# Kernel optimization log

Hardware: AMD Instinct MI355X
Metric: run time of the kernel (lower is better)

## Reference

```python
import jax, jax.numpy as jnp
import numpy as np

B, N, D_MODEL, N_HEADS = 4, 2048, 1024, 16
D_K = D_MODEL // N_HEADS  # 64


def setup_inputs() -> dict:
    key = jax.random.key(0)
    ks = jax.random.split(key, 7)
    s = 1.0 / np.sqrt(D_MODEL)
    return {
        "Q": jax.random.normal(ks[0], (B, N, D_MODEL), jnp.float32),
        "K": jax.random.normal(ks[1], (B, N, D_MODEL), jnp.float32),
        "V": jax.random.normal(ks[2], (B, N, D_MODEL), jnp.float32),
        "w_q": jax.random.normal(ks[3], (D_MODEL, D_MODEL), jnp.float32) * s,
        "w_k": jax.random.normal(ks[4], (D_MODEL, D_K), jnp.float32) * s,
        "w_v": jax.random.normal(ks[5], (D_MODEL, D_K), jnp.float32) * s,
        "w_o": jax.random.normal(ks[6], (D_MODEL, D_MODEL), jnp.float32) * s,
    }


def reference(Q, K, V, w_q, w_k, w_v, w_o):
    b, n, _ = Q.shape
    # projections: multi-query -> single shared K/V head of width d_k
    q = (Q @ w_q).reshape(b, n, N_HEADS, D_K)   # [b, n, h, d]
    k = K @ w_k                                  # [b, n, d]
    v = V @ w_v                                  # [b, n, d]
    scale = 1.0 / jnp.sqrt(jnp.asarray(D_K, q.dtype))
    scores = jnp.einsum("bnhd,bmd->bhnm", q, k) * scale  # [b, h, n, n]
    # causal mask: query i attends to keys j <= i (strictly-upper positions masked)
    causal = jnp.triu(jnp.ones((n, n), dtype=bool), k=1)
    scores = jnp.where(causal[None, None], -jnp.inf, scores)
    weights = jax.nn.softmax(scores, axis=-1)
    attn = jnp.einsum("bhnm,bmd->bnhd", weights, v).reshape(b, n, D_MODEL)
    return attn @ w_o
```

## Files before the change

### kernel.cpp

```cpp
#include <hip/hip_runtime.h>

typedef __bf16 bf16;
typedef unsigned int u32;
typedef __bf16 bf16x8 __attribute__((ext_vector_type(8)));
typedef float f32x4 __attribute__((ext_vector_type(4)));
typedef float f32x16 __attribute__((ext_vector_type(16)));

#define DEV __device__ __forceinline__

DEV void gload_lds16(const void* g, void* l) {
  __builtin_amdgcn_global_load_lds((const __attribute__((address_space(1))) void*)g,
                                   (__attribute__((address_space(3))) void*)l,
                                   16, 0, 0);
}

DEV u32 pack2(float a, float b) {
  unsigned short ua = __builtin_bit_cast(unsigned short, (bf16)a);
  unsigned short ub = __builtin_bit_cast(unsigned short, (bf16)b);
  return (u32)ua | ((u32)ub << 16);
}

__global__ void transpose_all(const float* __restrict__ wq, const float* __restrict__ wk,
                              const float* __restrict__ wv, const float* __restrict__ wo,
                              bf16* __restrict__ wqT, bf16* __restrict__ wkvT,
                              bf16* __restrict__ woT, float scale_q) {
  __shared__ float tile[32][33];
  int x = blockIdx.x;
  const float* in;
  bf16* out;
  int C;
  float scale = 1.0f;
  int c0;
  if (x < 32)      { in = wq; out = wqT;             C = 1024; c0 = x * 32; scale = scale_q; }
  else if (x < 34) { in = wk; out = wkvT;            C = 64;   c0 = (x - 32) * 32; }
  else if (x < 36) { in = wv; out = wkvT + 64 * 1024; C = 64;  c0 = (x - 34) * 32; }
  else             { in = wo; out = woT;             C = 1024; c0 = (x - 36) * 32; }
  int r0 = blockIdx.y * 32;
  int tx = threadIdx.x & 31, ty = threadIdx.x >> 5;
  for (int i = ty; i < 32; i += 8) tile[i][tx] = in[(size_t)(r0 + i) * C + c0 + tx];
  __syncthreads();
  for (int i = ty; i < 32; i += 8)
    out[(size_t)(c0 + i) * 1024 + r0 + tx] = (bf16)(tile[tx][i] * scale);
}

template <typename OutT>
__global__ __launch_bounds__(256)
void gemm_bt(const bf16* __restrict__ A, const bf16* __restrict__ Bt,
             OutT* __restrict__ C, int M, int N, int K) {
  __shared__ __align__(16) bf16 As[2][128 * 32];
  __shared__ __align__(16) bf16 Bs[2][128 * 32];
  const int tid = threadIdx.x;
  const int wid = tid >> 6, lane = tid & 63;
  const int wr = wid >> 1, wc = wid & 1;
  const int lx = lane & 15, g = lane >> 4;
  const size_t bm = (size_t)blockIdx.x * 128;
  const size_t bn = (size_t)blockIdx.y * 128;
  f32x4 acc[4][4] = {};
  const int nk = K >> 5;

  auto stage = [&](int buf, int k0) {
#pragma unroll
    for (int i = 0; i < 2; ++i) {
      int c = i * 256 + wid * 64 + lane;
      const bf16* gp = A + (bm + (size_t)(c >> 2)) * K + k0 + (c & 3) * 8;
      gload_lds16(gp, (char*)As[buf] + (size_t)(i * 256 + wid * 64) * 16);
    }
#pragma unroll
    for (int i = 0; i < 2; ++i) {
      int c = i * 256 + wid * 64 + lane;
      const bf16* gp = Bt + (bn + (size_t)(c >> 2)) * K + k0 + (c & 3) * 8;
      gload_lds16(gp, (char*)Bs[buf] + (size_t)(i * 256 + wid * 64) * 16);
    }
  };

  stage(0, 0);
  __syncthreads();
  int cur = 0;

  for (int t = 0; t < nk; ++t) {
    if (t + 1 < nk) stage(cur ^ 1, (t + 1) * 32);

    bf16x8 af[4], bfr[4];
#pragma unroll
    for (int m = 0; m < 4; ++m)
      af[m] = *(const bf16x8*)&As[cur][(wr * 64 + m * 16 + lx) * 32 + g * 8];
#pragma unroll
    for (int n = 0; n < 4; ++n)
      bfr[n] = *(const bf16x8*)&Bs[cur][(wc * 64 + n * 16 + lx) * 32 + g * 8];
#pragma unroll
    for (int m = 0; m < 4; ++m)
#pragma unroll
      for (int n = 0; n < 4; ++n)
        acc[m][n] = __builtin_amdgcn_mfma_f32_16x16x32_bf16(af[m], bfr[n], acc[m][n], 0, 0, 0);

    __syncthreads();
    cur ^= 1;
  }

#pragma unroll
  for (int m = 0; m < 4; ++m)
#pragma unroll
    for (int n = 0; n < 4; ++n) {
      size_t row = bm + wr * 64 + m * 16 + g * 4;
      size_t col = bn + wc * 64 + n * 16 + lx;
#pragma unroll
      for (int j = 0; j < 4; ++j)
        C[(row + j) * N + col] = (OutT)acc[m][n][j];
    }
}

__global__ __launch_bounds__(256)
void proj_kernel(const float* __restrict__ Qf, const float* __restrict__ Kf,
                 const float* __restrict__ Vf, const bf16* __restrict__ wqT,
                 const bf16* __restrict__ wkvT, bf16* __restrict__ qp,
                 bf16* __restrict__ kp, bf16* __restrict__ vTp) {
  const int bid = blockIdx.x;
  const bool isq = bid < 512;
  const float* Af;
  size_t arow, bm, bn;
  const bf16* Bt = isq ? wqT : wkvT;
  if (isq) {
    bm = (size_t)(bid & 63) * 128;
    arow = bm;
    bn = (size_t)(bid >> 6) * 128;
    Af = Qf;
  } else {
    int kv = bid - 512;
    bm = (size_t)kv * 128;
    bn = 0;
    if (kv < 64) { Af = Kf; arow = bm; } else { Af = Vf; arow = bm - 8192; }
  }

  __shared__ __align__(16) bf16 As[2][128 * 32];
  __shared__ __align__(16) bf16 Bs[2][128 * 32];
  const int tid = threadIdx.x;
  const int wid = tid >> 6, lane = tid & 63;
  const int wr = wid >> 1, wc = wid & 1;
  const int lx = lane & 15, g = lane >> 4;
  f32x4 acc[4][4] = {};

  auto loadA = [&](int k0, float4 (&ar)[2][2]) {
#pragma unroll
    for (int i = 0; i < 2; ++i) {
      int c = i * 256 + tid;
      const float* src = Af + (arow + (size_t)(c >> 2)) * 1024 + k0 + (c & 3) * 8;
      ar[i][0] = *(const float4*)src;
      ar[i][1] = *(const float4*)(src + 4);
    }
  };
  auto writeA = [&](int buf, const float4 (&ar)[2][2]) {
#pragma unroll
    for (int i = 0; i < 2; ++i) {
      bf16x8 v;
      v[0] = (bf16)ar[i][0].x; v[1] = (bf16)ar[i][0].y;
      v[2] = (bf16)ar[i][0].z; v[3] = (bf16)ar[i][0].w;
      v[4] = (bf16)ar[i][1].x; v[5] = (bf16)ar[i][1].y;
      v[6] = (bf16)ar[i][1].z; v[7] = (bf16)ar[i][1].w;
      *(bf16x8*)((char*)As[buf] + (size_t)(i * 256 + tid) * 16) = v;
    }
  };
  auto stageB = [&](int buf, int k0) {
#pragma unroll
    for (int i = 0; i < 2; ++i) {
      int c = i * 256 + wid * 64 + lane;
      const bf16* gp = Bt + (bn + (size_t)(c >> 2)) * 1024 + k0 + (c & 3) * 8;
      gload_lds16(gp, (char*)Bs[buf] + (size_t)(i * 256 + wid * 64) * 16);
    }
  };

  {
    float4 ar[2][2];
    loadA(0, ar);
    stageB(0, 0);
    writeA(0, ar);
  }
  __syncthreads();
  int cur = 0;

  for (int t = 0; t < 32; ++t) {
    float4 ar[2][2];
    const bool more = t + 1 < 32;
    if (more) {
      loadA((t + 1) * 32, ar);
      stageB(cur ^ 1, (t + 1) * 32);
    }

    bf16x8 af[4], bfr[4];
#pragma unroll
    for (int m = 0; m < 4; ++m)
      af[m] = *(const bf16x8*)&As[cur][(wr * 64 + m * 16 + lx) * 32 + g * 8];
#pragma unroll
    for (int n = 0; n < 4; ++n)
      bfr[n] = *(const bf16x8*)&Bs[cur][(wc * 64 + n * 16 + lx) * 32 + g * 8];
#pragma unroll
    for (int m = 0; m < 4; ++m)
#pragma unroll
      for (int n = 0; n < 4; ++n)
        acc[m][n] = __builtin_amdgcn_mfma_f32_16x16x32_bf16(af[m], bfr[n], acc[m][n], 0, 0, 0);

    if (more) writeA(cur ^ 1, ar);

    __syncthreads();
    cur ^= 1;
  }

#pragma unroll
  for (int m = 0; m < 4; ++m)
#pragma unroll
    for (int n = 0; n < 4; ++n) {
      size_t row = bm + wr * 64 + m * 16 + g * 4;
      size_t col = bn + wc * 64 + n * 16 + lx;
#pragma unroll
      for (int j = 0; j < 4; ++j) {
        float v = acc[m][n][j];
        size_t r = row + j;
        if (isq) {
          qp[r * 1024 + col] = (bf16)v;
        } else if (col < 64) {
          if (r < 8192) kp[r * 64 + col] = (bf16)v;
        } else {
          if (r >= 8192) {
            size_t rr = r - 8192;
            size_t bb = rr >> 11, nn = rr & 2047;
            vTp[bb * 131072 + (nn >> 5) * 2048 + (col - 64) * 32 + (nn & 31)] = (bf16)v;
          }
        }
      }
    }
}

__global__ __launch_bounds__(256, 2)
void attn_kernel(const bf16* __restrict__ q, const bf16* __restrict__ k,
                 const bf16* __restrict__ vt, bf16* __restrict__ o) {
  const int hg = blockIdx.y, b = blockIdx.z;
  const int wid = threadIdx.x >> 6, lane = threadIdx.x & 63;
  const int lq = lane & 31, hi = lane >> 5;
  const int h = hg * 4 + wid;
  const int pairIdx = blockIdx.x;

  __shared__ __align__(16) char Ks[2][8192];
  __shared__ __align__(16) char Vs[2][8192];
  __shared__ float bc[4][32];

  const bf16* kb = k + (size_t)b * 2048 * 64;
  const char* vbase = (const char*)vt + (size_t)b * 262144;

  auto stageK = [&](int bi, int kt, int sub) {
    int src = (wid * 64 + lane) ^ ((lane >> 3) & 7);
    gload_lds16((const char*)(kb + (size_t)kt * 2048) + src * 16,
                &Ks[bi][sub * 4096 + wid * 1024]);
  };
  auto stageV = [&](int bi, int kt, int sub) {
    int g = wid * 64 + lane;
    int src = (g & ~3) | ((g & 3) ^ ((lane >> 3) & 3));
    gload_lds16(vbase + (size_t)kt * 4096 + src * 16, &Vs[bi][sub * 4096 + wid * 1024]);
  };

  bf16x8 qf[4];

  auto qkt = [&](int cur, int sub) -> f32x16 {
    bf16x8 kf[4];
#pragma unroll
    for (int i = 0; i < 4; ++i)
      kf[i] = *(const bf16x8*)&Ks[cur][sub * 4096 + ((lq * 8 + i * 2 + hi) ^ (lq & 7)) * 16];
    f32x16 S = {};
#pragma unroll
    for (int i = 0; i < 4; ++i)
      S = __builtin_amdgcn_mfma_f32_32x32x16_bf16(kf[i], qf[i], S, 0, 0, 0);
    return S;
  };
  auto loadV = [&](int cur, int sub, bf16x8 (&vf)[2][2]) {
#pragma unroll
    for (int d = 0; d < 2; ++d)
#pragma unroll
      for (int ks = 0; ks < 2; ++ks)
        vf[d][ks] = *(const bf16x8*)&Vs[cur][sub * 4096 +
                        ((d * 32 + lq) * 4 + ((ks * 2 + hi) ^ ((lq >> 1) & 3))) * 16];
  };
  auto rebuild = [&](const u32 w[8], bf16x8& o0, bf16x8& o1) {
    u32 sw0 = (u32)__shfl_xor((int)w[0], 32), sw1 = (u32)__shfl_xor((int)w[1], 32);
    u32 sw2 = (u32)__shfl_xor((int)w[2], 32), sw3 = (u32)__shfl_xor((int)w[3], 32);
    u32 sw4 = (u32)__shfl_xor((int)w[4], 32), sw5 = (u32)__shfl_xor((int)w[5], 32);
    u32 sw6 = (u32)__shfl_xor((int)w[6], 32), sw7 = (u32)__shfl_xor((int)w[7], 32);
    union { u32 d[4]; bf16x8 v; } f0, f1;
    f0.d[0] = hi ? sw2 : w[0];
    f0.d[1] = hi ? sw3 : w[1];
    f0.d[2] = hi ? w[2] : sw0;
    f0.d[3] = hi ? w[3] : sw1;
    f1.d[0] = hi ? sw6 : w[4];
    f1.d[1] = hi ? sw7 : w[5];
    f1.d[2] = hi ? w[6] : sw4;
    f1.d[3] = hi ? w[7] : sw5;
    o0 = f0.v;
    o1 = f1.v;
  };

#pragma unroll 1
  for (int rep = 0; rep < 2; ++rep) {
    const int strip = rep ? pairIdx : 63 - pairIdx;
    const int qb = strip * 32;
    const int nt = strip + 1;
    const int nfull = nt >> 1, tail = nt & 1;

    const bf16* qrow = q + (size_t)(b * 2048 + qb + lq) * 1024 + h * 64 + hi * 8;
#pragma unroll
    for (int i = 0; i < 4; ++i) qf[i] = *(const bf16x8*)(qrow + i * 16);

    f32x16 O0 = {}, O1 = {};
    float m = -__builtin_inff(), l = 0.f;

    __syncthreads();
    if (nfull) {
      stageK(0, 0, 0); stageK(0, 1, 1);
      stageV(0, 0, 0); stageV(0, 1, 1);
    } else {
      stageK(0, 0, 0); stageV(0, 0, 0);
    }
    __syncthreads();
    int cur = 0;

    for (int r2 = 0; r2 < nfull; ++r2) {
      if (r2 + 1 < nfull) {
        stageK(cur ^ 1, 2 * r2 + 2, 0); stageK(cur ^ 1, 2 * r2 + 3, 1);
        stageV(cur ^ 1, 2 * r2 + 2, 0); stageV(cur ^ 1, 2 * r2 + 3, 1);
      } else if (tail) {
        stageK(cur ^ 1, 2 * nfull, 0); stageV(cur ^ 1, 2 * nfull, 0);
      }

      __builtin_amdgcn_s_setprio(1);
      f32x16 SA = qkt(cur, 0);
      f32x16 SB = qkt(cur, 1);
      __builtin_amdgcn_s_setprio(0);

      if (r2 == nfull - 1 && !tail) {
#pragma unroll
        for (int r = 0; r < 16; ++r) {
          int kr = (r & 3) + 8 * (r >> 2) + 4 * hi;
          if (kr > lq) SB[r] = -__builtin_inff();
        }
      }

      float pm = fmaxf(fmaxf(SA[0], SA[1]), SA[2]);
      pm = fmaxf(fmaxf(pm, SA[3]), SA[4]);
      pm = fmaxf(fmaxf(pm, SA[5]), SA[6]);
      pm = fmaxf(fmaxf(pm, SA[7]), SA[8]);
      pm = fmaxf(fmaxf(pm, SA[9]), SA[10]);
      pm = fmaxf(fmaxf(pm, SA[11]), SA[12]);
      pm = fmaxf(fmaxf(pm, SA[13]), SA[14]);
      pm = fmaxf(fmaxf(pm, SA[15]), SB[0]);
      pm = fmaxf(fmaxf(pm, SB[1]), SB[2]);
      pm = fmaxf(fmaxf(pm, SB[3]), SB[4]);
      pm = fmaxf(fmaxf(pm, SB[5]), SB[6]);
      pm = fmaxf(fmaxf(pm, SB[7]), SB[8]);
      pm = fmaxf(fmaxf(pm, SB[9]), SB[10]);
      pm = fmaxf(fmaxf(pm, SB[11]), SB[12]);
      pm = fmaxf(fmaxf(pm, SB[13]), SB[14]);
      pm = fmaxf(pm, SB[15]);
      pm = fmaxf(pm, __shfl_xor(pm, 32));

      if (!__all(pm <= m + 8.0f)) {
        float mn = fmaxf(m, pm);
        float fac = __builtin_amdgcn_exp2f(m - mn);
        m = mn;
        l *= fac;
        if (hi == 0) bc[wid][lq] = fac;
        __threadfence_block();
#pragma unroll
        for (int r = 0; r < 16; ++r) {
          float fr = bc[wid][(r & 3) + 8 * (r >> 2) + 4 * hi];
          O0[r] *= fr;
          O1[r] *= fr;
        }
      }

      float lsA = 0.f, lsB = 0.f;
      u32 wA[8], wB[8];
#pragma unroll
      for (int i = 0; i < 8; ++i) {
        float e0 = __builtin_amdgcn_exp2f(SA[2 * i] - m);
        float e1 = __builtin_amdgcn_exp2f(SA[2 * i + 1] - m);
        lsA += e0 + e1;
        wA[i] = pack2(e0, e1);
      }
#pragma unroll
      for (int i = 0; i < 8; ++i) {
        float e0 = __builtin_amdgcn_exp2f(SB[2 * i] - m);
        float e1 = __builtin_amdgcn_exp2f(SB[2 * i + 1] - m);
        lsB += e0 + e1;
        wB[i] = pack2(e0, e1);
      }
      float ls = lsA + lsB;
      ls += __shfl_xor(ls, 32);
      l += ls;

      bf16x8 f0A, f1A, f0B, f1B;
      rebuild(wA, f0A, f1A);
      rebuild(wB, f0B, f1B);

      bf16x8 vfA[2][2], vfB[2][2];
      loadV(cur, 0, vfA);
      loadV(cur, 1, vfB);

      __builtin_amdgcn_s_setprio(1);
      O0 = __builtin_amdgcn_mfma_f32_32x32x16_bf16(f0A, vfA[0][0], O0, 0, 0, 0);
      O0 = __builtin_amdgcn_mfma_f32_32x32x16_bf16(f1A, vfA[0][1], O0, 0, 0, 0);
      O0 = __builtin_amdgcn_mfma_f32_32x32x16_bf16(f0B, vfB[0][0], O0, 0, 0, 0);
      O0 = __builtin_amdgcn_mfma_f32_32x32x16_bf16(f1B, vfB[0][1], O0, 0, 0, 0);
      O1 = __builtin_amdgcn_mfma_f32_32x32x16_bf16(f0A, vfA[1][0], O1, 0, 0, 0);
      O1 = __builtin_amdgcn_mfma_f32_32x32x16_bf16(f1A, vfA[1][1], O1, 0, 0, 0);
      O1 = __builtin_amdgcn_mfma_f32_32x32x16_bf16(f0B, vfB[1][0], O1, 0, 0, 0);
      O1 = __builtin_amdgcn_mfma_f32_32x32x16_bf16(f1B, vfB[1][1], O1, 0, 0, 0);
      __builtin_amdgcn_s_setprio(0);

      __syncthreads();
      cur ^= 1;
    }

    if (tail) {
      __builtin_amdgcn_s_setprio(1);
      f32x16 S = qkt(cur, 0);
      __builtin_amdgcn_s_setprio(0);
#pragma unroll
      for (int r = 0; r < 16; ++r) {
        int kr = (r & 3) + 8 * (r >> 2) + 4 * hi;
        if (kr > lq) S[r] = -__builtin_inff();
      }
      float pm = fmaxf(fmaxf(S[0], S[1]), S[2]);
      pm = fmaxf(fmaxf(pm, S[3]), S[4]);
      pm = fmaxf(fmaxf(pm, S[5]), S[6]);
      pm = fmaxf(fmaxf(pm, S[7]), S[8]);
      pm = fmaxf(fmaxf(pm, S[9]), S[10]);
      pm = fmaxf(fmaxf(pm, S[11]), S[12]);
      pm = fmaxf(fmaxf(pm, S[13]), S[14]);
      pm = fmaxf(pm, S[15]);
      pm = fmaxf(pm, __shfl_xor(pm, 32));

      if (!__all(pm <= m + 8.0f)) {
        float mn = fmaxf(m, pm);
        float fac = __builtin_amdgcn_exp2f(m - mn);
        m = mn;
        l *= fac;
        if (hi == 0) bc[wid][lq] = fac;
        __threadfence_block();
#pragma unroll
        for (int r = 0; r < 16; ++r) {
          float fr = bc[wid][(r & 3) + 8 * (r >> 2) + 4 * hi];
          O0[r] *= fr;
          O1[r] *= fr;
        }
      }

      float ls = 0.f;
      u32 w[8];
#pragma unroll
      for (int i = 0; i < 8; ++i) {
        float e0 = __builtin_amdgcn_exp2f(S[2 * i] - m);
        float e1 = __builtin_amdgcn_exp2f(S[2 * i + 1] - m);
        ls += e0 + e1;
        w[i] = pack2(e0, e1);
      }
      ls += __shfl_xor(ls, 32);
      l += ls;

      bf16x8 f0, f1;
      rebuild(w, f0, f1);
      bf16x8 vf[2][2];
      loadV(cur, 0, vf);

      __builtin_amdgcn_s_setprio(1);
      O0 = __builtin_amdgcn_mfma_f32_32x32x16_bf16(f0, vf[0][0], O0, 0, 0, 0);
      O0 = __builtin_amdgcn_mfma_f32_32x32x16_bf16(f1, vf[0][1], O0, 0, 0, 0);
      O1 = __builtin_amdgcn_mfma_f32_32x32x16_bf16(f0, vf[1][0], O1, 0, 0, 0);
      O1 = __builtin_amdgcn_mfma_f32_32x32x16_bf16(f1, vf[1][1], O1, 0, 0, 0);
      __builtin_amdgcn_s_setprio(0);
    }

    float linv = 1.0f / l;
    if (hi == 0) bc[wid][lq] = linv;
    __threadfence_block();
#pragma unroll
    for (int r = 0; r < 16; ++r) {
      int row = (r & 3) + 8 * (r >> 2) + 4 * hi;
      float sc = bc[wid][row];
      size_t base = (size_t)(b * 2048 + qb + row) * 1024 + h * 64;
      o[base + lq] = (bf16)(O0[r] * sc);
      o[base + 32 + lq] = (bf16)(O1[r] * sc);
    }
  }
}

extern "C" void kernel_launch(void* const* d_in, const int* in_sizes, int n_in,
                              void* d_out, int out_size, void* d_ws, size_t ws_size,
                              hipStream_t stream) {
  const float* Q  = (const float*)d_in[0];
  const float* K  = (const float*)d_in[1];
  const float* V  = (const float*)d_in[2];
  const float* wq = (const float*)d_in[3];
  const float* wk = (const float*)d_in[4];
  const float* wv = (const float*)d_in[5];
  const float* wo = (const float*)d_in[6];
  float* out = (float*)d_out;

  char* ws = (char*)d_ws;
  bf16* qp   = (bf16*)(ws + (48ull << 20));
  bf16* ab   = (bf16*)(ws + (64ull << 20));
  bf16* kp   = (bf16*)(ws + (80ull << 20));
  bf16* vTp  = (bf16*)(ws + (81ull << 20));
  bf16* wqT  = (bf16*)(ws + (82ull << 20));
  bf16* woT  = (bf16*)(ws + (84ull << 20));
  bf16* wkvT = (bf16*)(ws + (86ull << 20));

  const float SCALE = 0.125f * 1.44269504088896340736f;
  transpose_all<<<dim3(68, 32), 256, 0, stream>>>(wq, wk, wv, wo, wqT, wkvT, woT, SCALE);

  proj_kernel<<<640, 256, 0, stream>>>(Q, K, V, wqT, wkvT, qp, kp, vTp);

  attn_kernel<<<dim3(32, 4, 4), 256, 0, stream>>>(qp, kp, vTp, ab);

  gemm_bt<float><<<dim3(64, 8), 256, 0, stream>>>(ab, woT, out, 8192, 1024, 1024);
}
```

Before: 153.7 us.

## Shrink attention blocks to two waves and broadcast rescale factors via shuffles

Attention blocks now hold 2 waves (2 heads) instead of 4, so the grid has twice as many blocks and each wave stages two 16-byte chunks of K and V into LDS. The per-row rescale and 1/l factors are broadcast with lane shuffles instead of going through a shared-memory array and a block fence. More blocks per CU may improve occupancy and load balance across the causal work. The cost is that each staged K/V tile is reused by fewer heads, which doubles global K/V traffic per head group.

```diff
diff --git a/kernel.cpp b/kernel.cpp
--- a/kernel.cpp
+++ b/kernel.cpp
@@ -229,31 +229,37 @@
     }
 }
 
-__global__ __launch_bounds__(256, 2)
+__global__ __launch_bounds__(128, 4)
 void attn_kernel(const bf16* __restrict__ q, const bf16* __restrict__ k,
                  const bf16* __restrict__ vt, bf16* __restrict__ o) {
   const int hg = blockIdx.y, b = blockIdx.z;
   const int wid = threadIdx.x >> 6, lane = threadIdx.x & 63;
   const int lq = lane & 31, hi = lane >> 5;
-  const int h = hg * 4 + wid;
+  const int h = hg * 2 + wid;
   const int pairIdx = blockIdx.x;
 
   __shared__ __align__(16) char Ks[2][8192];
   __shared__ __align__(16) char Vs[2][8192];
-  __shared__ float bc[4][32];
 
   const bf16* kb = k + (size_t)b * 2048 * 64;
   const char* vbase = (const char*)vt + (size_t)b * 262144;
 
   auto stageK = [&](int bi, int kt, int sub) {
-    int src = (wid * 64 + lane) ^ ((lane >> 3) & 7);
-    gload_lds16((const char*)(kb + (size_t)kt * 2048) + src * 16,
-                &Ks[bi][sub * 4096 + wid * 1024]);
+#pragma unroll
+    for (int i = 0; i < 2; ++i) {
+      int src = (i * 128 + wid * 64 + lane) ^ ((lane >> 3) & 7);
+      gload_lds16((const char*)(kb + (size_t)kt * 2048) + src * 16,
+                  &Ks[bi][sub * 4096 + (i * 2 + wid) * 1024]);
+    }
   };
   auto stageV = [&](int bi, int kt, int sub) {
-    int g = wid * 64 + lane;
-    int src = (g & ~3) | ((g & 3) ^ ((lane >> 3) & 3));
-    gload_lds16(vbase + (size_t)kt * 4096 + src * 16, &Vs[bi][sub * 4096 + wid * 1024]);
+#pragma unroll
+    for (int i = 0; i < 2; ++i) {
+      int gg = i * 128 + wid * 64 + lane;
+      int src = (gg & ~3) | ((gg & 3) ^ ((lane >> 3) & 3));
+      gload_lds16(vbase + (size_t)kt * 4096 + src * 16,
+                  &Vs[bi][sub * 4096 + (i * 2 + wid) * 1024]);
+    }
   };
 
   bf16x8 qf[4];
@@ -363,11 +369,9 @@
         float fac = __builtin_amdgcn_exp2f(m - mn);
         m = mn;
         l *= fac;
-        if (hi == 0) bc[wid][lq] = fac;
-        __threadfence_block();
 #pragma unroll
         for (int r = 0; r < 16; ++r) {
-          float fr = bc[wid][(r & 3) + 8 * (r >> 2) + 4 * hi];
+          float fr = __shfl(fac, (r & 3) + 8 * (r >> 2) + 4 * hi);
           O0[r] *= fr;
           O1[r] *= fr;
         }
@@ -440,11 +444,9 @@
         float fac = __builtin_amdgcn_exp2f(m - mn);
         m = mn;
         l *= fac;
-        if (hi == 0) bc[wid][lq] = fac;
-        __threadfence_block();
 #pragma unroll
         for (int r = 0; r < 16; ++r) {
-          float fr = bc[wid][(r & 3) + 8 * (r >> 2) + 4 * hi];
+          float fr = __shfl(fac, (r & 3) + 8 * (r >> 2) + 4 * hi);
           O0[r] *= fr;
           O1[r] *= fr;
         }
@@ -476,12 +478,10 @@
     }
 
     float linv = 1.0f / l;
-    if (hi == 0) bc[wid][lq] = linv;
-    __threadfence_block();
 #pragma unroll
     for (int r = 0; r < 16; ++r) {
       int row = (r & 3) + 8 * (r >> 2) + 4 * hi;
-      float sc = bc[wid][row];
+      float sc = __shfl(linv, row);
       size_t base = (size_t)(b * 2048 + qb + row) * 1024 + h * 64;
       o[base + lq] = (bf16)(O0[r] * sc);
       o[base + 32 + lq] = (bf16)(O1[r] * sc);
@@ -515,7 +515,7 @@
 
   proj_kernel<<<640, 256, 0, stream>>>(Q, K, V, wqT, wkvT, qp, kp, vTp);
 
-  attn_kernel<<<dim3(32, 4, 4), 256, 0, stream>>>(qp, kp, vTp, ab);
+  attn_kernel<<<dim3(32, 8, 4), 128, 0, stream>>>(qp, kp, vTp, ab);
 
   gemm_bt<float><<<dim3(64, 8), 256, 0, stream>>>(ab, woT, out, 8192, 1024, 1024);
 }
```

New measurement: 195.3 us. +27.1%, slower.
